# Kernel tuning notes

Measured on AMD Instinct MI355X. Metric: run time of the kernel, lower is better.

Reference implementation:

```python
import jax, jax.numpy as jnp
import numpy as np
from jax import lax

LBDA = 0.5   # soft-min temperature from OTAM_cum_dist_v2 default
EPS = 0.01   # cos_sim epsilon


def otam_cum_dist(dists, lbda=LBDA):
    """Soft-DTW-style OTAM DP. dists: [nq, ns, L, S] -> [nq, ns].
    Faithful to OTAM_cum_dist_v2: pad last dim by (1,1) with zeros, then run the
    row-wise recurrence. Soft-min computed via stable logsumexp (same math as
    -lbda*log(sum exp(-x/lbda)))."""
    nq, ns, L, S = dists.shape
    d = jnp.pad(dists, ((0, 0), (0, 0), (0, 0), (1, 1)))  # [nq, ns, L, W], W=S+2
    W = S + 2
    # Row 0: cum[0, m] = cum[0, m-1] + d[0, m], cum[0, 0] = 0
    row0 = jnp.concatenate(
        [jnp.zeros((nq, ns, 1), d.dtype), jnp.cumsum(d[:, :, 0, 1:], axis=-1)], axis=-1)
    if L == 1:
        return row0[..., -1]

    m_idx = jnp.arange(1, W)
    include_up = (m_idx == 1) | (m_idx == W - 1)  # only first/last cols use cum[l-1, m]
    INF = jnp.asarray(jnp.inf, d.dtype)

    def row_step(prev_row, d_row):
        # prev_row, d_row: [nq, ns, W]
        xs = (
            jnp.moveaxis(d_row[:, :, 1:], -1, 0),        # d[l, m],       [W-1, nq, ns]
            jnp.moveaxis(prev_row[:, :, :-1], -1, 0),    # cum[l-1, m-1]
            jnp.moveaxis(prev_row[:, :, 1:], -1, 0),     # cum[l-1, m]
            include_up,
        )

        def col_step(cur_left, x):
            d_m, p_diag, p_up, inc = x
            up = jnp.where(inc, p_up, INF)               # masked term -> exp(-inf)=0
            terms = jnp.stack([p_diag, cur_left, up])    # [3, nq, ns]
            new = d_m - lbda * jax.nn.logsumexp(-terms / lbda, axis=0)
            return new, new

        _, cols = lax.scan(col_step, jnp.zeros((nq, ns), d.dtype), xs)
        row = jnp.concatenate(
            [jnp.zeros((nq, ns, 1), d.dtype), jnp.moveaxis(cols, 0, -1)], axis=-1)
        return row, None

    d_rows = jnp.moveaxis(d[:, :, 1:, :], 2, 0)          # [L-1, nq, ns, W]
    final_row, _ = lax.scan(row_step, row0, d_rows)
    return final_row[..., -1]


def reference(support_features, query_features):
    """OTAM meta-logits (cum_dist_g = -otam_distance) of DSN_TEMPORAL.
    support_features: [n_classes, L, D] class prototypes; query_features: [nq, L, D]."""
    nq, Lq, D = query_features.shape
    ns, Ls, _ = support_features.shape
    q = query_features.reshape(nq * Lq, D)
    s = support_features.reshape(ns * Ls, D)
    # cos_sim with epsilon in denominator (faithful to cos_sim())
    num = q @ s.T
    den = (jnp.linalg.norm(q, axis=-1)[:, None]
           * jnp.linalg.norm(s, axis=-1)[None, :] + EPS)
    frame_dists = 1.0 - num / den                         # [nq*L, ns*S]
    dists = frame_dists.reshape(nq, Lq, ns, Ls).transpose(0, 2, 1, 3)  # [nq, ns, L, S]
    cum = otam_cum_dist(dists) + otam_cum_dist(dists.transpose(0, 1, 3, 2))
    return -cum                                           # meta_logits [nq, ns]


def setup_inputs() -> dict:
    key = jax.random.key(0)
    k1, k2 = jax.random.split(key)
    return {
        "support_features": jax.random.normal(k1, (64, 8, 576), dtype=jnp.float32),
        "query_features": jax.random.normal(k2, (2048, 8, 576), dtype=jnp.float32),
    }
```

## Files before the change

### kernel.cpp

```cpp
#include <hip/hip_runtime.h>

#define D_K 576
#define NSLAB 18
#define LBDA_INV 2.0f
#define HALF_LBDA 0.5f
#define EPS 0.01f
#define DSTRIDE 136

#define NQROW 16384
#define NSROW 512
#define NQT 128
#define NST 4
#define NT 132
#define TILE_ELEMS (128 * D_K)
#define SLAB_ELEMS (128 * 32)

typedef __attribute__((ext_vector_type(8))) short short8;
typedef __attribute__((ext_vector_type(4))) short short4v;
typedef __attribute__((ext_vector_type(4))) float f32x4;

__device__ inline short f2bf(float f) {
    unsigned u = __float_as_uint(f);
    u += 0x7FFF + ((u >> 16) & 1);
    return (short)(u >> 16);
}
__device__ inline float bf2f(unsigned short s) {
    return __uint_as_float(((unsigned)s) << 16);
}

__global__ __launch_bounds__(256) void prep_kernel(
        const float* __restrict__ sup, const float* __restrict__ qry,
        unsigned short* __restrict__ tb, float* __restrict__ psum) {
    __shared__ unsigned short Ls[SLAB_ELEMS];
    const int t = threadIdx.x;
    const int slab = blockIdx.x;
    const int tile = blockIdx.y;
    const bool isq = tile < NQT;
    const float* src = (isq ? qry + (size_t)tile * 128 * D_K
                            : sup + (size_t)(tile - NQT) * 128 * D_K) + slab * 32;
    float* ps = psum + ((size_t)tile * NSLAB + slab) * 128;

#pragma unroll
    for (int i = 0; i < 4; ++i) {
        int idx = i * 256 + t;
        int r = idx >> 3, c = idx & 7;
        float4 v = *(const float4*)(src + (size_t)r * D_K + c * 4);
        float ss = v.x * v.x + v.y * v.y + v.z * v.z + v.w * v.w;
        ss += __shfl_down(ss, 4);
        ss += __shfl_down(ss, 2);
        ss += __shfl_down(ss, 1);
        if ((t & 7) == 0) ps[r] = ss;
        int c_in = c >> 1, half = c & 1;
        short4v o = {f2bf(v.x), f2bf(v.y), f2bf(v.z), f2bf(v.w)};
        *(short4v*)(&Ls[(c_in * 128 + r) * 8 + half * 4]) = o;
    }
    __syncthreads();
    unsigned short* dst = tb + (size_t)tile * TILE_ELEMS + (size_t)slab * SLAB_ELEMS;
    *(short8*)(dst + t * 16) = *(const short8*)(&Ls[t * 16]);
    *(short8*)(dst + t * 16 + 8) = *(const short8*)(&Ls[t * 16 + 8]);
}

__device__ inline float softmin3(float a, float b, float c) {
    float mn = fminf(a, fminf(b, c));
    float s = __expf(-LBDA_INV * (a - mn)) + __expf(-LBDA_INV * (b - mn)) +
              __expf(-LBDA_INV * (c - mn));
    return mn - HALF_LBDA * __logf(s);
}
__device__ inline float softmin2(float a, float b) {
    float mn = fminf(a, b);
    float s = __expf(-LBDA_INV * (a - mn)) + __expf(-LBDA_INV * (b - mn));
    return mn - HALF_LBDA * __logf(s);
}

template <int RS, int CS>
__device__ float otam_dp(const float* d) {
    float prev[10], cur[10];
    prev[0] = 0.f;
#pragma unroll
    for (int m = 1; m <= 8; ++m) prev[m] = prev[m - 1] + d[0 * RS + (m - 1) * CS];
    prev[9] = prev[8];
#pragma unroll
    for (int l = 1; l < 8; ++l) {
        cur[0] = 0.f;
        cur[1] = d[l * RS + 0 * CS] + softmin3(prev[0], 0.f, prev[1]);
#pragma unroll
        for (int m = 2; m <= 8; ++m)
            cur[m] = d[l * RS + (m - 1) * CS] + softmin2(prev[m - 1], cur[m - 1]);
        cur[9] = softmin3(prev[8], cur[8], prev[9]);
#pragma unroll
        for (int m = 0; m < 10; ++m) prev[m] = cur[m];
    }
    return prev[9];
}

__global__ __launch_bounds__(256, 2) void fused_kernel(
        const unsigned short* __restrict__ tb, const float* __restrict__ psum,
        float* __restrict__ out) {
    __shared__ unsigned short Ds[128 * DSTRIDE];
    __shared__ float qn_l[128], sn_l[128];

    const int t = threadIdx.x;
    const int b = blockIdx.x;
    const int xcd = b & 7, s2 = b >> 3;
    const int sblk = s2 >> 4;
    const int qblk = xcd * 16 + (s2 & 15);

    {
        const float* pq = psum + (size_t)qblk * NSLAB * 128;
        const float* ps = psum + (size_t)(NQT + sblk) * NSLAB * 128;
        if (t < 128) {
            float a = 0.f;
#pragma unroll
            for (int sl = 0; sl < NSLAB; ++sl) a += pq[sl * 128 + t];
            qn_l[t] = sqrtf(a);
        } else {
            int r = t - 128;
            float a = 0.f;
#pragma unroll
            for (int sl = 0; sl < NSLAB; ++sl) a += ps[sl * 128 + r];
            sn_l[r] = sqrtf(a);
        }
    }

    const unsigned short* At = tb + (size_t)qblk * TILE_ELEMS;
    const unsigned short* Bt = tb + (size_t)(NQT + sblk) * TILE_ELEMS;

    const int lane = t & 63;
    const int wave = t >> 6;
    const int wm = wave >> 1, wn = wave & 1;
    const int col16 = lane & 15, quad = lane >> 4;

    f32x4 acc[4][4];
#pragma unroll
    for (int i = 0; i < 4; ++i)
#pragma unroll
        for (int j = 0; j < 4; ++j) acc[i][j] = (f32x4){0.f, 0.f, 0.f, 0.f};

    int aoff[4], boff[4];
#pragma unroll
    for (int mt = 0; mt < 4; ++mt)
        aoff[mt] = (quad * 128 + wm * 64 + mt * 16 + col16) * 8;
#pragma unroll
    for (int nt = 0; nt < 4; ++nt)
        boff[nt] = (quad * 128 + wn * 64 + nt * 16 + col16) * 8;

#pragma unroll 3
    for (int sl = 0; sl < NSLAB; ++sl) {
        const unsigned short* Asl = At + sl * SLAB_ELEMS;
        const unsigned short* Bsl = Bt + sl * SLAB_ELEMS;
        short8 af[4], bf[4];
#pragma unroll
        for (int mt = 0; mt < 4; ++mt) af[mt] = *(const short8*)(Asl + aoff[mt]);
#pragma unroll
        for (int nt = 0; nt < 4; ++nt) bf[nt] = *(const short8*)(Bsl + boff[nt]);
#pragma unroll
        for (int mt = 0; mt < 4; ++mt)
#pragma unroll
            for (int nt = 0; nt < 4; ++nt)
                acc[mt][nt] = __builtin_amdgcn_mfma_f32_16x16x32_bf16(
                    af[mt], bf[nt], acc[mt][nt], 0, 0, 0);
    }
    __syncthreads();

#pragma unroll
    for (int mt = 0; mt < 4; ++mt) {
#pragma unroll
        for (int reg = 0; reg < 4; ++reg) {
            int m = wm * 64 + mt * 16 + quad * 4 + reg;
            float qv = qn_l[m];
#pragma unroll
            for (int nt = 0; nt < 4; ++nt) {
                int n = wn * 64 + nt * 16 + col16;
                float sv = sn_l[n];
                float dist = 1.f - acc[mt][nt][reg] / (qv * sv + EPS);
                Ds[m * DSTRIDE + n] = (unsigned short)f2bf(dist);
            }
        }
    }
    __syncthreads();

    const int ql = t >> 4, sl = t & 15;
    float d[64];
#pragma unroll
    for (int l = 0; l < 8; ++l) {
        short8 rowv = *(const short8*)(&Ds[(ql * 8 + l) * DSTRIDE + sl * 8]);
#pragma unroll
        for (int j = 0; j < 8; ++j) d[l * 8 + j] = bf2f((unsigned short)rowv[j]);
    }
    float r1 = otam_dp<8, 1>(d);
    float r2 = otam_dp<1, 8>(d);
    int qg = qblk * 16 + ql, sg = sblk * 16 + sl;
    out[qg * 64 + sg] = -(r1 + r2);
}

extern "C" void kernel_launch(void* const* d_in, const int* in_sizes, int n_in,
                              void* d_out, int out_size, void* d_ws, size_t ws_size,
                              hipStream_t stream) {
    const float* sup = (const float*)d_in[0];
    const float* qry = (const float*)d_in[1];
    float* out = (float*)d_out;

    unsigned short* tb = (unsigned short*)d_ws;
    float* psum = (float*)(tb + (size_t)NT * TILE_ELEMS);

    prep_kernel<<<dim3(NSLAB, NT), dim3(256), 0, stream>>>(sup, qry, tb, psum);
    fused_kernel<<<dim3(512), dim3(256), 0, stream>>>(tb, psum, out);
}
```

Before: 111.9 us.

## Fuse bf16 conversion and norm computation into the main kernel with double-buffered LDS

Drops the separate prep kernel and its workspace round-trip. The fused kernel now loads fp32 query and support slabs straight from global memory, converts them to bf16 and accumulates squared norms in registers. It writes the slabs into double-buffered, XOR-swizzled shared memory while MFMAs run on the previous slab. This saves one launch and the write/read of the bf16 tiles, but each block re-reads and re-converts fp32 inputs (support tiles are shared by many blocks), adds a barrier per slab, and raises LDS use, which may cut occupancy. The divide is also replaced by a reciprocal multiply.

```diff
diff --git a/kernel.cpp b/kernel.cpp
--- a/kernel.cpp
+++ b/kernel.cpp
@@ -6,14 +6,7 @@
 #define HALF_LBDA 0.5f
 #define EPS 0.01f
 #define DSTRIDE 136
-
-#define NQROW 16384
-#define NSROW 512
-#define NQT 128
-#define NST 4
-#define NT 132
-#define TILE_ELEMS (128 * D_K)
-#define SLAB_ELEMS (128 * 32)
+#define SLAB_USHORTS 4096
 
 typedef __attribute__((ext_vector_type(8))) short short8;
 typedef __attribute__((ext_vector_type(4))) short short4v;
@@ -26,38 +19,6 @@
 }
 __device__ inline float bf2f(unsigned short s) {
     return __uint_as_float(((unsigned)s) << 16);
-}
-
-__global__ __launch_bounds__(256) void prep_kernel(
-        const float* __restrict__ sup, const float* __restrict__ qry,
-        unsigned short* __restrict__ tb, float* __restrict__ psum) {
-    __shared__ unsigned short Ls[SLAB_ELEMS];
-    const int t = threadIdx.x;
-    const int slab = blockIdx.x;
-    const int tile = blockIdx.y;
-    const bool isq = tile < NQT;
-    const float* src = (isq ? qry + (size_t)tile * 128 * D_K
-                            : sup + (size_t)(tile - NQT) * 128 * D_K) + slab * 32;
-    float* ps = psum + ((size_t)tile * NSLAB + slab) * 128;
-
-#pragma unroll
-    for (int i = 0; i < 4; ++i) {
-        int idx = i * 256 + t;
-        int r = idx >> 3, c = idx & 7;
-        float4 v = *(const float4*)(src + (size_t)r * D_K + c * 4);
-        float ss = v.x * v.x + v.y * v.y + v.z * v.z + v.w * v.w;
-        ss += __shfl_down(ss, 4);
-        ss += __shfl_down(ss, 2);
-        ss += __shfl_down(ss, 1);
-        if ((t & 7) == 0) ps[r] = ss;
-        int c_in = c >> 1, half = c & 1;
-        short4v o = {f2bf(v.x), f2bf(v.y), f2bf(v.z), f2bf(v.w)};
-        *(short4v*)(&Ls[(c_in * 128 + r) * 8 + half * 4]) = o;
-    }
-    __syncthreads();
-    unsigned short* dst = tb + (size_t)tile * TILE_ELEMS + (size_t)slab * SLAB_ELEMS;
-    *(short8*)(dst + t * 16) = *(const short8*)(&Ls[t * 16]);
-    *(short8*)(dst + t * 16 + 8) = *(const short8*)(&Ls[t * 16 + 8]);
 }
 
 __device__ inline float softmin3(float a, float b, float c) {
@@ -94,8 +55,10 @@
 }
 
 __global__ __launch_bounds__(256, 2) void fused_kernel(
-        const unsigned short* __restrict__ tb, const float* __restrict__ psum,
+        const float* __restrict__ sup, const float* __restrict__ qry,
         float* __restrict__ out) {
+    __shared__ unsigned short As[2][SLAB_USHORTS];
+    __shared__ unsigned short Bs[2][SLAB_USHORTS];
     __shared__ unsigned short Ds[128 * DSTRIDE];
     __shared__ float qn_l[128], sn_l[128];
 
@@ -105,25 +68,12 @@
     const int sblk = s2 >> 4;
     const int qblk = xcd * 16 + (s2 & 15);
 
-    {
-        const float* pq = psum + (size_t)qblk * NSLAB * 128;
-        const float* ps = psum + (size_t)(NQT + sblk) * NSLAB * 128;
-        if (t < 128) {
-            float a = 0.f;
-#pragma unroll
-            for (int sl = 0; sl < NSLAB; ++sl) a += pq[sl * 128 + t];
-            qn_l[t] = sqrtf(a);
-        } else {
-            int r = t - 128;
-            float a = 0.f;
-#pragma unroll
-            for (int sl = 0; sl < NSLAB; ++sl) a += ps[sl * 128 + r];
-            sn_l[r] = sqrtf(a);
-        }
-    }
-
-    const unsigned short* At = tb + (size_t)qblk * TILE_ELEMS;
-    const unsigned short* Bt = tb + (size_t)(NQT + sblk) * TILE_ELEMS;
+    const float* qsrc = qry + (size_t)qblk * 128 * D_K;
+    const float* ssrc = sup + (size_t)sblk * 128 * D_K;
+
+    const int rr = t >> 3;
+    const int cc = t & 7;
+    const int c_in = cc >> 1, half = cc & 1;
 
     const int lane = t & 63;
     const int wave = t >> 6;
@@ -136,29 +86,83 @@
 #pragma unroll
         for (int j = 0; j < 4; ++j) acc[i][j] = (f32x4){0.f, 0.f, 0.f, 0.f};
 
-    int aoff[4], boff[4];
+    int aoff[4], boff[4], woff[4];
 #pragma unroll
     for (int mt = 0; mt < 4; ++mt)
-        aoff[mt] = (quad * 128 + wm * 64 + mt * 16 + col16) * 8;
+        aoff[mt] = (quad * 128 + ((wm * 64 + mt * 16 + col16) ^ (quad << 1))) * 8;
 #pragma unroll
     for (int nt = 0; nt < 4; ++nt)
-        boff[nt] = (quad * 128 + wn * 64 + nt * 16 + col16) * 8;
-
-#pragma unroll 3
+        boff[nt] = (quad * 128 + ((wn * 64 + nt * 16 + col16) ^ (quad << 1))) * 8;
+#pragma unroll
+    for (int i = 0; i < 4; ++i)
+        woff[i] = (c_in * 128 + ((i * 32 + rr) ^ (c_in << 1))) * 8 + half * 4;
+
+    float ssA[4] = {0.f, 0.f, 0.f, 0.f}, ssB[4] = {0.f, 0.f, 0.f, 0.f};
+    float4 va[4], vb[4];
+
+#pragma unroll
+    for (int i = 0; i < 4; ++i) {
+        va[i] = *(const float4*)(qsrc + (size_t)(i * 32 + rr) * D_K + cc * 4);
+        vb[i] = *(const float4*)(ssrc + (size_t)(i * 32 + rr) * D_K + cc * 4);
+    }
+#pragma unroll
+    for (int i = 0; i < 4; ++i) {
+        ssA[i] += va[i].x * va[i].x + va[i].y * va[i].y + va[i].z * va[i].z + va[i].w * va[i].w;
+        ssB[i] += vb[i].x * vb[i].x + vb[i].y * vb[i].y + vb[i].z * vb[i].z + vb[i].w * vb[i].w;
+        short4v oa = {f2bf(va[i].x), f2bf(va[i].y), f2bf(va[i].z), f2bf(va[i].w)};
+        short4v ob = {f2bf(vb[i].x), f2bf(vb[i].y), f2bf(vb[i].z), f2bf(vb[i].w)};
+        *(short4v*)(&As[0][woff[i]]) = oa;
+        *(short4v*)(&Bs[0][woff[i]]) = ob;
+    }
+    __syncthreads();
+
+#pragma unroll
     for (int sl = 0; sl < NSLAB; ++sl) {
-        const unsigned short* Asl = At + sl * SLAB_ELEMS;
-        const unsigned short* Bsl = Bt + sl * SLAB_ELEMS;
-        short8 af[4], bf[4];
-#pragma unroll
-        for (int mt = 0; mt < 4; ++mt) af[mt] = *(const short8*)(Asl + aoff[mt]);
-#pragma unroll
-        for (int nt = 0; nt < 4; ++nt) bf[nt] = *(const short8*)(Bsl + boff[nt]);
+        const int cur = sl & 1;
+        const bool more = (sl + 1) < NSLAB;
+        if (more) {
+            const int off = (sl + 1) * 32 + cc * 4;
+#pragma unroll
+            for (int i = 0; i < 4; ++i) {
+                va[i] = *(const float4*)(qsrc + (size_t)(i * 32 + rr) * D_K + off);
+                vb[i] = *(const float4*)(ssrc + (size_t)(i * 32 + rr) * D_K + off);
+            }
+        }
+        short8 af[4], bq[4];
+#pragma unroll
+        for (int mt = 0; mt < 4; ++mt) af[mt] = *(const short8*)(&As[cur][aoff[mt]]);
+#pragma unroll
+        for (int nt = 0; nt < 4; ++nt) bq[nt] = *(const short8*)(&Bs[cur][boff[nt]]);
 #pragma unroll
         for (int mt = 0; mt < 4; ++mt)
 #pragma unroll
             for (int nt = 0; nt < 4; ++nt)
                 acc[mt][nt] = __builtin_amdgcn_mfma_f32_16x16x32_bf16(
-                    af[mt], bf[nt], acc[mt][nt], 0, 0, 0);
+                    af[mt], bq[nt], acc[mt][nt], 0, 0, 0);
+        if (more) {
+            const int nb = cur ^ 1;
+#pragma unroll
+            for (int i = 0; i < 4; ++i) {
+                ssA[i] += va[i].x * va[i].x + va[i].y * va[i].y + va[i].z * va[i].z + va[i].w * va[i].w;
+                ssB[i] += vb[i].x * vb[i].x + vb[i].y * vb[i].y + vb[i].z * vb[i].z + vb[i].w * vb[i].w;
+                short4v oa = {f2bf(va[i].x), f2bf(va[i].y), f2bf(va[i].z), f2bf(va[i].w)};
+                short4v ob = {f2bf(vb[i].x), f2bf(vb[i].y), f2bf(vb[i].z), f2bf(vb[i].w)};
+                *(short4v*)(&As[nb][woff[i]]) = oa;
+                *(short4v*)(&Bs[nb][woff[i]]) = ob;
+            }
+        }
+        __syncthreads();
+    }
+
+#pragma unroll
+    for (int i = 0; i < 4; ++i) {
+        float a = ssA[i], s = ssB[i];
+        a += __shfl_down(a, 4); a += __shfl_down(a, 2); a += __shfl_down(a, 1);
+        s += __shfl_down(s, 4); s += __shfl_down(s, 2); s += __shfl_down(s, 1);
+        if ((t & 7) == 0) {
+            qn_l[i * 32 + rr] = sqrtf(a);
+            sn_l[i * 32 + rr] = sqrtf(s);
+        }
     }
     __syncthreads();
 
@@ -172,24 +176,24 @@
             for (int nt = 0; nt < 4; ++nt) {
                 int n = wn * 64 + nt * 16 + col16;
                 float sv = sn_l[n];
-                float dist = 1.f - acc[mt][nt][reg] / (qv * sv + EPS);
+                float dist = 1.f - acc[mt][nt][reg] * __builtin_amdgcn_rcpf(qv * sv + EPS);
                 Ds[m * DSTRIDE + n] = (unsigned short)f2bf(dist);
             }
         }
     }
     __syncthreads();
 
-    const int ql = t >> 4, sl = t & 15;
+    const int ql = t >> 4, sj = t & 15;
     float d[64];
 #pragma unroll
     for (int l = 0; l < 8; ++l) {
-        short8 rowv = *(const short8*)(&Ds[(ql * 8 + l) * DSTRIDE + sl * 8]);
+        short8 rowv = *(const short8*)(&Ds[(ql * 8 + l) * DSTRIDE + sj * 8]);
 #pragma unroll
         for (int j = 0; j < 8; ++j) d[l * 8 + j] = bf2f((unsigned short)rowv[j]);
     }
     float r1 = otam_dp<8, 1>(d);
     float r2 = otam_dp<1, 8>(d);
-    int qg = qblk * 16 + ql, sg = sblk * 16 + sl;
+    int qg = qblk * 16 + ql, sg = sblk * 16 + sj;
     out[qg * 64 + sg] = -(r1 + r2);
 }
 
@@ -199,10 +203,6 @@
     const float* sup = (const float*)d_in[0];
     const float* qry = (const float*)d_in[1];
     float* out = (float*)d_out;
-
-    unsigned short* tb = (unsigned short*)d_ws;
-    float* psum = (float*)(tb + (size_t)NT * TILE_ELEMS);
-
-    prep_kernel<<<dim3(NSLAB, NT), dim3(256), 0, stream>>>(sup, qry, tb, psum);
-    fused_kernel<<<dim3(512), dim3(256), 0, stream>>>(tb, psum, out);
-}
+    (void)d_ws; (void)ws_size;
+    fused_kernel<<<dim3(512), dim3(256), 0, stream>>>(sup, qry, out);
+}
```

Measured after the change: 257.0 us. 2.3x slower.
